# Optimization experiments

Measured on AMD Instinct MI355X. Metric: run time of the kernel, lower is better.

## Reference

```python
import jax, jax.numpy as jnp
import numpy as np


def setup_inputs() -> dict:
    key = jax.random.key(0)
    ks = jax.random.split(key, 6)
    B, T, D, H = 2, 2048, 1024, 16
    dk = D // H
    s = 0.02
    return {
        "x": jax.random.normal(ks[0], (B, T, D), dtype=jnp.float32),
        "Wq": jax.random.normal(ks[1], (H, dk, dk), dtype=jnp.float32) * s,
        "Wk": jax.random.normal(ks[2], (H, dk, dk), dtype=jnp.float32) * s,
        "Wv": jax.random.normal(ks[3], (H, dk, dk), dtype=jnp.float32) * s,
        "Wp": jax.random.normal(ks[4], (D, D), dtype=jnp.float32) * s,
        "bp": jnp.zeros((D,), dtype=jnp.float32),
    }


def reference(x, Wq, Wk, Wv, Wp, bp):
    B, T, D = x.shape
    H, dk, _ = Wq.shape
    # split into heads: [B, H, T, dk]
    xh = x.reshape(B, T, H, dk).transpose(0, 2, 1, 3)
    # per-head torch Linear (y = x @ W^T), all heads at once
    q = jnp.einsum('bhtd,hkd->bhtk', xh, Wq)
    k = jnp.einsum('bhtd,hkd->bhtk', xh, Wk)
    v = jnp.einsum('bhtd,hkd->bhtk', xh, Wv)
    scale = 1.0 / jnp.sqrt(jnp.float32(dk))  # original divides by sqrt(C) with C == d_k
    scores = jnp.einsum('bhqd,bhkd->bhqk', q, k) * scale
    causal = jnp.tril(jnp.ones((T, T), dtype=bool))
    scores = jnp.where(causal[None, None], scores, -jnp.inf)
    attn = jax.nn.softmax(scores, axis=-1)
    out = jnp.einsum('bhqk,bhkd->bhqd', attn, v)  # [B,H,T,dk]
    out = out.transpose(0, 2, 1, 3).reshape(B, T, D)  # concat heads
    return out @ Wp.T + bp
```

## Files before the change

kernel.cpp:

```cpp
#include <hip/hip_runtime.h>
#include <math.h>

#define B_ 2
#define T_ 2048
#define D_ 1024
#define H_ 16
#define DK 64
#define BH_ (B_*H_)

typedef __attribute__((ext_vector_type(8))) short short8;
typedef __attribute__((ext_vector_type(4))) short bf16x4;
typedef __attribute__((ext_vector_type(4))) float fragC;

#if defined(__HIP_DEVICE_COMPILE__)
#define MFMA16(A,B,C) __builtin_amdgcn_mfma_f32_16x16x16bf16_1k((A),(B),(C),0,0,0)
#else
#define MFMA16(A,B,C) (C)
#endif
#define MFMA32(A,B,C) __builtin_amdgcn_mfma_f32_16x16x32_bf16((A),(B),(C),0,0,0)

__device__ __forceinline__ unsigned short f2bf(float x) {
    union { float f; unsigned u; } c; c.f = x;
    unsigned r = c.u + 0x7fff + ((c.u >> 16) & 1);
    return (unsigned short)(r >> 16);
}

__device__ __forceinline__ unsigned pack2bf(float a, float b) {
    return (unsigned)f2bf(a) | ((unsigned)f2bf(b) << 16);
}

__device__ __forceinline__ unsigned permpack(float a, float b) {
    union { float f; unsigned u; } ca, cb; ca.f = a; cb.f = b;
    return __builtin_amdgcn_perm(cb.u, ca.u, 0x07060302);
}

__device__ __forceinline__ short8 packbf8(float4 a, float4 b) {
    union { short8 v; unsigned u[4]; } r;
    r.u[0] = pack2bf(a.x, a.y); r.u[1] = pack2bf(a.z, a.w);
    r.u[2] = pack2bf(b.x, b.y); r.u[3] = pack2bf(b.z, b.w);
    return r.v;
}

__device__ __forceinline__ void gload_lds16(const void* g, void* l) {
    __builtin_amdgcn_global_load_lds(
        (const __attribute__((address_space(1))) unsigned int*)g,
        (__attribute__((address_space(3))) unsigned int*)l, 16, 0, 0);
}

__global__ __launch_bounds__(256) void cvt_kernel(
    const float* __restrict__ Wp,
    const float* __restrict__ Wq, const float* __restrict__ Wk,
    const float* __restrict__ Wv,
    unsigned short* __restrict__ Wb, unsigned short* __restrict__ wqkvb)
{
    const int gid = blockIdx.x * 256 + threadIdx.x;
    const float* src; unsigned short* dst;
    if (gid < 131072) { src = Wp + (size_t)gid * 8; dst = Wb + (size_t)gid * 8; }
    else              { int e = gid - 131072;
                        int mat = e >> 13, rem = e & 8191;
                        int h = rem >> 9, od = rem & 511;
                        const float* ws = (mat == 0) ? Wq : (mat == 1) ? Wk : Wv;
                        src = ws + ((size_t)(h << 9) + od) * 8;
                        dst = wqkvb + ((size_t)h*1536 + mat*512 + od) * 8; }
    float4 a = *(const float4*)src;
    float4 b = *(const float4*)(src + 4);
    *(uint4*)dst = make_uint4(pack2bf(a.x, a.y), pack2bf(a.z, a.w),
                              pack2bf(b.x, b.y), pack2bf(b.z, b.w));
}

__global__ __launch_bounds__(256) void qkv_kernel(
    const float* __restrict__ x,
    const unsigned short* __restrict__ wqkvb,
    unsigned short* __restrict__ q, unsigned short* __restrict__ k,
    unsigned short* __restrict__ vt)
{
    __shared__ unsigned short Wl[3*64*64];

    const int bh = blockIdx.x;
    const int b  = bh >> 4, h = bh & 15;
    const int t0 = blockIdx.y * 64;
    const int tid = threadIdx.x;
    const int wave = tid >> 6, lane = tid & 63;
    const int n = lane & 15, quad = lane >> 4;

    {
        const unsigned short* wsrc = wqkvb + (size_t)h * 12288;
        #pragma unroll
        for (int j = 0; j < 6; ++j) {
            const int off = (wave*6 + j) * 512 + lane*8;
            gload_lds16(wsrc + off, &Wl[off]);
        }
    }

    const int tw = t0 + wave*16;
    short8 xf[2];
    {
        const float* xr = &x[((size_t)b*T_ + tw + n)*D_ + h*DK];
        float4 a0 = *(const float4*)&xr[quad*8];
        float4 a1 = *(const float4*)&xr[quad*8 + 4];
        xf[0] = packbf8(a0, a1);
        float4 b0 = *(const float4*)&xr[32 + quad*8];
        float4 b1 = *(const float4*)&xr[32 + quad*8 + 4];
        xf[1] = packbf8(b0, b1);
    }
    __syncthreads();

    const float qsc = 0.125f * 1.44269504088896340736f;
    const int tb0 = blockIdx.y*4 + wave;
    const int ktv = tw >> 6, ctv = (tw >> 4) & 3;
    #pragma unroll
    for (int mat = 0; mat < 3; ++mat) {
        const int wbase = mat * 4096;
        #pragma unroll
        for (int ct = 0; ct < 4; ++ct) {
            short8 wf0 = *(const short8*)&Wl[wbase + (ct*16 + n)*64 + quad*8];
            short8 wf1 = *(const short8*)&Wl[wbase + (ct*16 + n)*64 + 32 + quad*8];
            fragC z = {0.f,0.f,0.f,0.f};
            if (mat < 2) {
                z = MFMA32(wf0, xf[0], z);
                z = MFMA32(wf1, xf[1], z);
                if (mat == 0) {
                    z[0] *= qsc; z[1] *= qsc; z[2] *= qsc; z[3] *= qsc;
                }
                unsigned short* dstg = (mat == 0) ? q : k;
                unsigned short* dp = &dstg[((size_t)bh*128 + tb0)*1024
                                           + (ct*2 + (quad>>1))*128 + n*8 + (quad&1)*4];
                *(uint2*)dp = make_uint2(pack2bf(z[0], z[1]), pack2bf(z[2], z[3]));
            } else {
                z = MFMA32(xf[0], wf0, z);
                z = MFMA32(xf[1], wf1, z);
                unsigned short* dp = &vt[(size_t)bh*131072 + ktv*4096
                                         + ct*1024 + ctv*256 + quad*64 + n*4];
                *(uint2*)dp = make_uint2(pack2bf(z[0], z[1]), pack2bf(z[2], z[3]));
            }
        }
    }
}

__global__ __launch_bounds__(256, 4) void attn_kernel(
    const unsigned short* __restrict__ q, const unsigned short* __restrict__ k,
    const unsigned short* __restrict__ vt, unsigned short* __restrict__ aout)
{
    __shared__ unsigned short Ks[2][4096];
    __shared__ unsigned short Vs[2][4096];

    const int id = blockIdx.x;
    const int bh = id >> 4;
    const int e  = id & 15;

    const int b   = bh >> 4, h = bh & 15;
    const int tid = threadIdx.x;
    const int wave = tid >> 6, lane = tid & 63;
    const int n = lane & 15, quad = lane >> 4;

    bf16x4 ones4;
    #pragma unroll
    for (int j = 0; j < 4; ++j) ones4[j] = (short)0x3F80;

    const unsigned short* kg = &k[(size_t)bh*131072];
    const unsigned short* vg = &vt[(size_t)bh*131072];

    #pragma unroll
    for (int pass = 0; pass < 2; ++pass) {
        const int qt = pass ? (31 - e) : e;
        const int q0 = qt*64 + wave*16;
        const int nt = qt + 1;

        const unsigned short* qb = &q[((size_t)bh*128 + qt*4 + wave)*1024 + n*8];
        short8 qf0 = *(const short8*)&qb[quad*128];
        short8 qf1 = *(const short8*)&qb[(4 + quad)*128];

        fragC o[4];
        #pragma unroll
        for (int dt = 0; dt < 4; ++dt) o[dt] = (fragC){0.f,0.f,0.f,0.f};
        fragC l4 = {0.f,0.f,0.f,0.f};

        if (pass) __syncthreads();
        gload_lds16(kg + tid*8,        &Ks[0][tid*8]);
        gload_lds16(kg + 2048 + tid*8, &Ks[0][2048 + tid*8]);
        gload_lds16(vg + tid*8,        &Vs[0][tid*8]);
        gload_lds16(vg + 2048 + tid*8, &Vs[0][2048 + tid*8]);

        for (int kt = 0; kt < nt; ++kt) {
            __syncthreads();
            if (kt + 1 < nt) {
                const int nb = (kt + 1) & 1;
                const unsigned short* kgn = kg + (size_t)(kt+1)*4096;
                const unsigned short* vgn = vg + (size_t)(kt+1)*4096;
                gload_lds16(kgn + tid*8,        &Ks[nb][tid*8]);
                gload_lds16(kgn + 2048 + tid*8, &Ks[nb][2048 + tid*8]);
                gload_lds16(vgn + tid*8,        &Vs[nb][tid*8]);
                gload_lds16(vgn + 2048 + tid*8, &Vs[nb][2048 + tid*8]);
            }
            const unsigned short* Kb = Ks[kt & 1];
            const unsigned short* Vb = Vs[kt & 1];
            const bool diag = (kt == qt);

            bf16x4 pp[4];
            #pragma unroll
            for (int ct = 0; ct < 4; ++ct) {
                short8 kf0 = *(const short8*)&Kb[ct*1024 + quad*128 + n*8];
                short8 kf1 = *(const short8*)&Kb[ct*1024 + 512 + quad*128 + n*8];
                fragC c = {0.f,0.f,0.f,0.f};
                c = MFMA32(kf0, qf0, c);
                c = MFMA32(kf1, qf1, c);
                float p0 = exp2f(c[0]), p1 = exp2f(c[1]);
                float p2 = exp2f(c[2]), p3 = exp2f(c[3]);
                if (diag) {
                    const int lim = (wave*16 + n) - (ct*16 + quad*4);
                    if (0 > lim) p0 = 0.f;
                    if (1 > lim) p1 = 0.f;
                    if (2 > lim) p2 = 0.f;
                    if (3 > lim) p3 = 0.f;
                }
                union { bf16x4 v; unsigned u[2]; } pk;
                pk.u[0] = permpack(p0, p1);
                pk.u[1] = permpack(p2, p3);
                pp[ct] = pk.v;
            }
            #pragma unroll
            for (int ct = 0; ct < 4; ++ct)
                l4 = MFMA16(ones4, pp[ct], l4);
            #pragma unroll
            for (int dt = 0; dt < 4; ++dt) {
                #pragma unroll
                for (int ct = 0; ct < 4; ++ct) {
                    bf16x4 vf = *(const bf16x4*)&Vb[dt*1024 + ct*256 + quad*64 + n*4];
                    o[dt] = MFMA16(vf, pp[ct], o[dt]);
                }
            }
        }

        const float inv = 1.0f / l4[0];
        unsigned short* dp = &aout[((size_t)b*T_ + q0 + n)*D_ + h*DK + quad*4];
        #pragma unroll
        for (int dt = 0; dt < 4; ++dt) {
            *(uint2*)(dp + dt*16) =
                make_uint2(pack2bf(o[dt][0]*inv, o[dt][1]*inv),
                           pack2bf(o[dt][2]*inv, o[dt][3]*inv));
        }
    }
}

__global__ __launch_bounds__(256) void proj_kernel(
    const unsigned short* __restrict__ A, const unsigned short* __restrict__ Wb,
    const float* __restrict__ bp, float* __restrict__ out)
{
    __shared__ unsigned short As[64*64];
    __shared__ unsigned short Bs[128*64];

    const int m0 = blockIdx.x * 64, n0 = blockIdx.y * 128;
    const int tid = threadIdx.x;
    const int wave = tid >> 6, lane = tid & 63;
    const int n = lane & 15, quad = lane >> 4;

    const int srowB = wave*32 + (lane >> 3);
    const int srowA = wave*16 + (lane >> 3);
    const int scol  = (lane & 7) * 8;
    const unsigned short* ag = &A [(size_t)(m0 + srowA)*1024 + scol];
    const unsigned short* bg = &Wb[(size_t)(n0 + srowB)*1024 + scol];
    unsigned short* al = &As[(size_t)srowA*64 + scol];
    unsigned short* bl = &Bs[(size_t)srowB*64 + scol];

    fragC acc[4][2];
    #pragma unroll
    for (int i = 0; i < 4; ++i)
        #pragma unroll
        for (int j = 0; j < 2; ++j) acc[i][j] = (fragC){0.f,0.f,0.f,0.f};

    for (int kt = 0; kt < 16; ++kt) {
        __syncthreads();
        #pragma unroll
        for (int i = 0; i < 2; ++i)
            gload_lds16(ag + (size_t)i*8*1024 + kt*64, al + i*8*64);
        #pragma unroll
        for (int i = 0; i < 4; ++i)
            gload_lds16(bg + (size_t)i*8*1024 + kt*64, bl + i*8*64);
        __syncthreads();

        #pragma unroll
        for (int kk = 0; kk < 2; ++kk) {
            short8 af[4], bf[2];
            #pragma unroll
            for (int i = 0; i < 4; ++i)
                af[i] = *(const short8*)&As[(i*16 + n)*64 + kk*32 + quad*8];
            #pragma unroll
            for (int j = 0; j < 2; ++j)
                bf[j] = *(const short8*)&Bs[(wave*32 + j*16 + n)*64 + kk*32 + quad*8];
            #pragma unroll
            for (int i = 0; i < 4; ++i)
                #pragma unroll
                for (int j = 0; j < 2; ++j)
                    acc[i][j] = MFMA32(af[i], bf[j], acc[i][j]);
        }
    }

    #pragma unroll
    for (int i = 0; i < 4; ++i) {
        #pragma unroll
        for (int r = 0; r < 4; ++r) {
            const int m = m0 + i*16 + quad*4 + r;
            #pragma unroll
            for (int j = 0; j < 2; ++j) {
                const int col = n0 + wave*32 + j*16 + n;
                out[(size_t)m*1024 + col] = acc[i][j][r] + bp[col];
            }
        }
    }
}

extern "C" void kernel_launch(void* const* d_in, const int* in_sizes, int n_in,
                              void* d_out, int out_size, void* d_ws, size_t ws_size,
                              hipStream_t stream)
{
    const float* x  = (const float*)d_in[0];
    const float* Wq = (const float*)d_in[1];
    const float* Wk = (const float*)d_in[2];
    const float* Wv = (const float*)d_in[3];
    const float* Wp = (const float*)d_in[4];
    const float* bp = (const float*)d_in[5];
    float* out = (float*)d_out;

    const size_t per = (size_t)BH_ * T_ * DK;
    unsigned short* qws   = (unsigned short*)d_ws;
    unsigned short* kws   = qws + per;
    unsigned short* vtws  = kws + per;
    unsigned short* aws   = vtws + per;
    unsigned short* wbws  = aws + per;
    unsigned short* wqkvb = wbws + 1024*1024;

    cvt_kernel<<<dim3(608), 256, 0, stream>>>(Wp, Wq, Wk, Wv, wbws, wqkvb);
    qkv_kernel<<<dim3(BH_, T_/64), 256, 0, stream>>>(x, wqkvb, qws, kws, vtws);
    attn_kernel<<<dim3(512), 256, 0, stream>>>(qws, kws, vtws, aws);
    proj_kernel<<<dim3(64, 8), 256, 0, stream>>>(aws, wbws, bp, out);
}
```

Baseline: 151.6 us.

## Process two query tiles per attention block and double qkv rows per block

Measured after the change: 150.6 us. About the same (-0.7%).

```diff
diff --git a/kernel.cpp b/kernel.cpp
--- a/kernel.cpp
+++ b/kernel.cpp
@@ -78,7 +78,7 @@
 
     const int bh = blockIdx.x;
     const int b  = bh >> 4, h = bh & 15;
-    const int t0 = blockIdx.y * 64;
+    const int t0 = blockIdx.y * 128;
     const int tid = threadIdx.x;
     const int wave = tid >> 6, lane = tid & 63;
     const int n = lane & 15, quad = lane >> 4;
@@ -92,22 +92,22 @@
         }
     }
 
-    const int tw = t0 + wave*16;
-    short8 xf[2];
-    {
-        const float* xr = &x[((size_t)b*T_ + tw + n)*D_ + h*DK];
+    const int tw = t0 + wave*32;
+    short8 xf[2][2];
+    #pragma unroll
+    for (int rt = 0; rt < 2; ++rt) {
+        const float* xr = &x[((size_t)b*T_ + tw + rt*16 + n)*D_ + h*DK];
         float4 a0 = *(const float4*)&xr[quad*8];
         float4 a1 = *(const float4*)&xr[quad*8 + 4];
-        xf[0] = packbf8(a0, a1);
+        xf[rt][0] = packbf8(a0, a1);
         float4 b0 = *(const float4*)&xr[32 + quad*8];
         float4 b1 = *(const float4*)&xr[32 + quad*8 + 4];
-        xf[1] = packbf8(b0, b1);
+        xf[rt][1] = packbf8(b0, b1);
     }
     __syncthreads();
 
     const float qsc = 0.125f * 1.44269504088896340736f;
-    const int tb0 = blockIdx.y*4 + wave;
-    const int ktv = tw >> 6, ctv = (tw >> 4) & 3;
+    const int tb0 = blockIdx.y*8 + wave*2;
     #pragma unroll
     for (int mat = 0; mat < 3; ++mat) {
         const int wbase = mat * 4096;
@@ -115,29 +115,34 @@
         for (int ct = 0; ct < 4; ++ct) {
             short8 wf0 = *(const short8*)&Wl[wbase + (ct*16 + n)*64 + quad*8];
             short8 wf1 = *(const short8*)&Wl[wbase + (ct*16 + n)*64 + 32 + quad*8];
-            fragC z = {0.f,0.f,0.f,0.f};
-            if (mat < 2) {
-                z = MFMA32(wf0, xf[0], z);
-                z = MFMA32(wf1, xf[1], z);
-                if (mat == 0) {
-                    z[0] *= qsc; z[1] *= qsc; z[2] *= qsc; z[3] *= qsc;
+            #pragma unroll
+            for (int rt = 0; rt < 2; ++rt) {
+                fragC z = {0.f,0.f,0.f,0.f};
+                if (mat < 2) {
+                    z = MFMA32(wf0, xf[rt][0], z);
+                    z = MFMA32(wf1, xf[rt][1], z);
+                    if (mat == 0) {
+                        z[0] *= qsc; z[1] *= qsc; z[2] *= qsc; z[3] *= qsc;
+                    }
+                    unsigned short* dstg = (mat == 0) ? q : k;
+                    unsigned short* dp = &dstg[((size_t)bh*128 + tb0 + rt)*1024
+                                               + (ct*2 + (quad>>1))*128 + n*8 + (quad&1)*4];
+                    *(uint2*)dp = make_uint2(pack2bf(z[0], z[1]), pack2bf(z[2], z[3]));
+                } else {
+                    z = MFMA32(xf[rt][0], wf0, z);
+                    z = MFMA32(xf[rt][1], wf1, z);
+                    const int key0 = tw + rt*16;
+                    const int ktv = key0 >> 6, ctv = (key0 >> 4) & 3;
+                    unsigned short* dp = &vt[(size_t)bh*131072 + ktv*4096
+                                             + ct*1024 + ctv*256 + quad*64 + n*4];
+                    *(uint2*)dp = make_uint2(pack2bf(z[0], z[1]), pack2bf(z[2], z[3]));
                 }
-                unsigned short* dstg = (mat == 0) ? q : k;
-                unsigned short* dp = &dstg[((size_t)bh*128 + tb0)*1024
-                                           + (ct*2 + (quad>>1))*128 + n*8 + (quad&1)*4];
-                *(uint2*)dp = make_uint2(pack2bf(z[0], z[1]), pack2bf(z[2], z[3]));
-            } else {
-                z = MFMA32(xf[0], wf0, z);
-                z = MFMA32(xf[1], wf1, z);
-                unsigned short* dp = &vt[(size_t)bh*131072 + ktv*4096
-                                         + ct*1024 + ctv*256 + quad*64 + n*4];
-                *(uint2*)dp = make_uint2(pack2bf(z[0], z[1]), pack2bf(z[2], z[3]));
             }
         }
     }
 }
 
-__global__ __launch_bounds__(256, 4) void attn_kernel(
+__global__ __launch_bounds__(256, 2) void attn_kernel(
     const unsigned short* __restrict__ q, const unsigned short* __restrict__ k,
     const unsigned short* __restrict__ vt, unsigned short* __restrict__ aout)
 {
@@ -145,14 +150,31 @@
     __shared__ unsigned short Vs[2][4096];
 
     const int id = blockIdx.x;
-    const int bh = id >> 4;
-    const int e  = id & 15;
+    int qt, bh;
+    if (id < 256) { bh = id >> 3;         qt = 15 - (id & 7); }
+    else          { bh = (id - 256) >> 3; qt = (id - 256) & 7; }
 
     const int b   = bh >> 4, h = bh & 15;
     const int tid = threadIdx.x;
     const int wave = tid >> 6, lane = tid & 63;
     const int n = lane & 15, quad = lane >> 4;
 
+    short8 qf[2][2];
+    #pragma unroll
+    for (int rt = 0; rt < 2; ++rt) {
+        const unsigned short* qb =
+            &q[((size_t)bh*128 + qt*8 + rt*4 + wave)*1024 + n*8];
+        qf[rt][0] = *(const short8*)&qb[quad*128];
+        qf[rt][1] = *(const short8*)&qb[(4 + quad)*128];
+    }
+
+    fragC o[2][4];
+    #pragma unroll
+    for (int rt = 0; rt < 2; ++rt)
+        #pragma unroll
+        for (int dt = 0; dt < 4; ++dt) o[rt][dt] = (fragC){0.f,0.f,0.f,0.f};
+    fragC l4[2] = {(fragC){0.f,0.f,0.f,0.f}, (fragC){0.f,0.f,0.f,0.f}};
+
     bf16x4 ones4;
     #pragma unroll
     for (int j = 0; j < 4; ++j) ones4[j] = (short)0x3F80;
@@ -160,41 +182,30 @@
     const unsigned short* kg = &k[(size_t)bh*131072];
     const unsigned short* vg = &vt[(size_t)bh*131072];
 
-    #pragma unroll
-    for (int pass = 0; pass < 2; ++pass) {
-        const int qt = pass ? (31 - e) : e;
-        const int q0 = qt*64 + wave*16;
-        const int nt = qt + 1;
-
-        const unsigned short* qb = &q[((size_t)bh*128 + qt*4 + wave)*1024 + n*8];
-        short8 qf0 = *(const short8*)&qb[quad*128];
-        short8 qf1 = *(const short8*)&qb[(4 + quad)*128];
-
-        fragC o[4];
-        #pragma unroll
-        for (int dt = 0; dt < 4; ++dt) o[dt] = (fragC){0.f,0.f,0.f,0.f};
-        fragC l4 = {0.f,0.f,0.f,0.f};
-
-        if (pass) __syncthreads();
-        gload_lds16(kg + tid*8,        &Ks[0][tid*8]);
-        gload_lds16(kg + 2048 + tid*8, &Ks[0][2048 + tid*8]);
-        gload_lds16(vg + tid*8,        &Vs[0][tid*8]);
-        gload_lds16(vg + 2048 + tid*8, &Vs[0][2048 + tid*8]);
-
-        for (int kt = 0; kt < nt; ++kt) {
-            __syncthreads();
-            if (kt + 1 < nt) {
-                const int nb = (kt + 1) & 1;
-                const unsigned short* kgn = kg + (size_t)(kt+1)*4096;
-                const unsigned short* vgn = vg + (size_t)(kt+1)*4096;
-                gload_lds16(kgn + tid*8,        &Ks[nb][tid*8]);
-                gload_lds16(kgn + 2048 + tid*8, &Ks[nb][2048 + tid*8]);
-                gload_lds16(vgn + tid*8,        &Vs[nb][tid*8]);
-                gload_lds16(vgn + 2048 + tid*8, &Vs[nb][2048 + tid*8]);
-            }
-            const unsigned short* Kb = Ks[kt & 1];
-            const unsigned short* Vb = Vs[kt & 1];
-            const bool diag = (kt == qt);
+    const int nt = 2*qt + 2;
+    gload_lds16(kg + tid*8,        &Ks[0][tid*8]);
+    gload_lds16(kg + 2048 + tid*8, &Ks[0][2048 + tid*8]);
+    gload_lds16(vg + tid*8,        &Vs[0][tid*8]);
+    gload_lds16(vg + 2048 + tid*8, &Vs[0][2048 + tid*8]);
+
+    for (int kt = 0; kt < nt; ++kt) {
+        __syncthreads();
+        if (kt + 1 < nt) {
+            const int nb = (kt + 1) & 1;
+            const unsigned short* kgn = kg + (size_t)(kt+1)*4096;
+            const unsigned short* vgn = vg + (size_t)(kt+1)*4096;
+            gload_lds16(kgn + tid*8,        &Ks[nb][tid*8]);
+            gload_lds16(kgn + 2048 + tid*8, &Ks[nb][2048 + tid*8]);
+            gload_lds16(vgn + tid*8,        &Vs[nb][tid*8]);
+            gload_lds16(vgn + 2048 + tid*8, &Vs[nb][2048 + tid*8]);
+        }
+        const unsigned short* Kb = Ks[kt & 1];
+        const unsigned short* Vb = Vs[kt & 1];
+
+        #pragma unroll
+        for (int rt = 0; rt < 2; ++rt) {
+            if (rt == 0 && kt == nt - 1) continue;
+            const bool diag = (kt == 2*qt + rt);
 
             bf16x4 pp[4];
             #pragma unroll
@@ -202,8 +213,8 @@
                 short8 kf0 = *(const short8*)&Kb[ct*1024 + quad*128 + n*8];
                 short8 kf1 = *(const short8*)&Kb[ct*1024 + 512 + quad*128 + n*8];
                 fragC c = {0.f,0.f,0.f,0.f};
-                c = MFMA32(kf0, qf0, c);
-                c = MFMA32(kf1, qf1, c);
+                c = MFMA32(kf0, qf[rt][0], c);
+                c = MFMA32(kf1, qf[rt][1], c);
                 float p0 = exp2f(c[0]), p1 = exp2f(c[1]);
                 float p2 = exp2f(c[2]), p3 = exp2f(c[3]);
                 if (diag) {
@@ -220,24 +231,28 @@
             }
             #pragma unroll
             for (int ct = 0; ct < 4; ++ct)
-                l4 = MFMA16(ones4, pp[ct], l4);
+                l4[rt] = MFMA16(ones4, pp[ct], l4[rt]);
             #pragma unroll
             for (int dt = 0; dt < 4; ++dt) {
                 #pragma unroll
                 for (int ct = 0; ct < 4; ++ct) {
                     bf16x4 vf = *(const bf16x4*)&Vb[dt*1024 + ct*256 + quad*64 + n*4];
-                    o[dt] = MFMA16(vf, pp[ct], o[dt]);
+                    o[rt][dt] = MFMA16(vf, pp[ct], o[rt][dt]);
                 }
             }
         }
-
-        const float inv = 1.0f / l4[0];
+    }
+
+    #pragma unroll
+    for (int rt = 0; rt < 2; ++rt) {
+        const int q0 = qt*128 + rt*64 + wave*16;
+        const float inv = 1.0f / l4[rt][0];
         unsigned short* dp = &aout[((size_t)b*T_ + q0 + n)*D_ + h*DK + quad*4];
         #pragma unroll
         for (int dt = 0; dt < 4; ++dt) {
             *(uint2*)(dp + dt*16) =
-                make_uint2(pack2bf(o[dt][0]*inv, o[dt][1]*inv),
-                           pack2bf(o[dt][2]*inv, o[dt][3]*inv));
+                make_uint2(pack2bf(o[rt][dt][0]*inv, o[rt][dt][1]*inv),
+                           pack2bf(o[rt][dt][2]*inv, o[rt][dt][3]*inv));
         }
     }
 }
@@ -330,7 +345,7 @@
     unsigned short* wqkvb = wbws + 1024*1024;
 
     cvt_kernel<<<dim3(608), 256, 0, stream>>>(Wp, Wq, Wk, Wv, wbws, wqkvb);
-    qkv_kernel<<<dim3(BH_, T_/64), 256, 0, stream>>>(x, wqkvb, qws, kws, vtws);
+    qkv_kernel<<<dim3(BH_, T_/128), 256, 0, stream>>>(x, wqkvb, qws, kws, vtws);
     attn_kernel<<<dim3(512), 256, 0, stream>>>(qws, kws, vtws, aws);
     proj_kernel<<<dim3(64, 8), 256, 0, stream>>>(aws, wbws, bp, out);
 }
```
